# Optimization experiments

Hardware: AMD Instinct MI355X
Metric: run time of the kernel (lower is better)

The kernel has to match this reference:

```python
import jax, jax.numpy as jnp
import numpy as np

NUM_HEADS = 16
HEAD_SIZE = 64
N_EMBD = 1024
BLOCK_SIZE = 2048
B, T = 4, 2048


def setup_inputs() -> dict:
    key = jax.random.key(0)
    ks = jax.random.split(key, 6)
    scale = (N_EMBD * NUM_HEADS) ** (-0.5)
    x = jax.random.normal(ks[0], (B, T, N_EMBD), dtype=jnp.float32)
    Wk = jax.random.normal(ks[1], (NUM_HEADS, N_EMBD, HEAD_SIZE), dtype=jnp.float32) * scale
    Wq = jax.random.normal(ks[2], (NUM_HEADS, N_EMBD, HEAD_SIZE), dtype=jnp.float32) * scale
    Wv = jax.random.normal(ks[3], (NUM_HEADS, N_EMBD, HEAD_SIZE), dtype=jnp.float32) * scale
    proj_w = jax.random.normal(ks[4], (N_EMBD, N_EMBD), dtype=jnp.float32) * (N_EMBD ** -0.5)
    proj_b = jax.random.normal(ks[5], (N_EMBD,), dtype=jnp.float32) * 0.01
    return {"x": x, "Wk": Wk, "Wq": Wq, "Wv": Wv, "proj_w": proj_w, "proj_b": proj_b}


def reference(x, Wk, Wq, Wv, proj_w, proj_b):
    Bsz, Tlen, C = x.shape
    # per-head projections: x [b,t,c] @ W [h,c,d] -> [b,h,t,d]
    q = jnp.einsum('btc,hcd->bhtd', x, Wq)
    k = jnp.einsum('btc,hcd->bhtd', x, Wk)
    v = jnp.einsum('btc,hcd->bhtd', x, Wv)
    wei = jnp.einsum('bhtd,bhsd->bhts', q, k) * (HEAD_SIZE ** -0.5)
    causal = jnp.tril(jnp.ones((Tlen, Tlen), dtype=bool))  # [T,T]
    wei = jnp.where(causal[None, None, :, :], wei, -jnp.inf)
    wei = jax.nn.softmax(wei, axis=-1)
    out = jnp.einsum('bhts,bhsd->bhtd', wei, v)
    out = out.transpose(0, 2, 1, 3).reshape(Bsz, Tlen, NUM_HEADS * HEAD_SIZE)
    out = out @ proj_w.T + proj_b  # nn.Linear: x W^T + b
    return out
```

## Files before the change

### kernel.cpp

```cpp
#include <hip/hip_runtime.h>
#include <hip/hip_bf16.h>

#define BB 4
#define TT 2048
#define CC 1024
#define HH 16
#define DD 64
#define MM (BB * TT)
#define NN_QKV 3072

typedef __attribute__((ext_vector_type(8))) short short8;
typedef __attribute__((ext_vector_type(4))) short short4v;
typedef __attribute__((ext_vector_type(4))) int i32x4;
typedef __attribute__((ext_vector_type(4))) float f32x4;
typedef __attribute__((ext_vector_type(16))) float f32x16;

static __device__ __forceinline__ float exp2_hw(float x) {
  return __builtin_amdgcn_exp2f(x);
}

static __device__ __forceinline__ short f2bf(float f) {
  __hip_bfloat16 h = __float2bfloat16(f);
  short s;
  __builtin_memcpy(&s, &h, 2);
  return s;
}

static __device__ __forceinline__ unsigned int pack2(float a, float b) {
  unsigned int lo = (unsigned short)f2bf(a);
  unsigned int hi = (unsigned short)f2bf(b);
  return lo | (hi << 16);
}

static __device__ __forceinline__ f32x16 zero16() {
  f32x16 z;
#pragma unroll
  for (int i = 0; i < 16; ++i) z[i] = 0.f;
  return z;
}

static __device__ __forceinline__ int swzv(int d) {
  return (((d & 7) ^ ((d >> 3) & 7)) << 4);
}

static __device__ __forceinline__ void gld16(const void* g, void* l) {
  __builtin_amdgcn_global_load_lds(
      (const __attribute__((address_space(1))) unsigned int*)g,
      (__attribute__((address_space(3))) unsigned int*)l, 16, 0, 0);
}

__global__ __launch_bounds__(256) void cvt8_kernel(const float* __restrict__ in,
                                                   short* __restrict__ out, int n8) {
  int i = blockIdx.x * 256 + threadIdx.x;
  if (i >= n8) return;
  const float4 a = ((const float4*)in)[i * 2];
  const float4 b = ((const float4*)in)[i * 2 + 1];
  short8 o;
  o[0] = f2bf(a.x); o[1] = f2bf(a.y); o[2] = f2bf(a.z); o[3] = f2bf(a.w);
  o[4] = f2bf(b.x); o[5] = f2bf(b.y); o[6] = f2bf(b.z); o[7] = f2bf(b.w);
  ((short8*)out)[i] = o;
}

__global__ __launch_bounds__(256) void cvtw_kernel(
    const float* __restrict__ Wq, const float* __restrict__ Wk,
    const float* __restrict__ Wv, short* __restrict__ Wt) {
  __shared__ float tile[64][65];
  const int tid = threadIdx.x;
  const int h = blockIdx.x;
  const int c0 = blockIdx.y * 64;
  const int sel = blockIdx.z;
  const float* W = (sel == 0) ? Wq : (sel == 1) ? Wk : Wv;

#pragma unroll
  for (int it = 0; it < 16; ++it) {
    int e = it * 256 + tid;
    int cc = e >> 6, d = e & 63;
    tile[d][cc] = W[((size_t)h * CC + c0 + cc) * DD + d];
  }
  __syncthreads();
#pragma unroll
  for (int it = 0; it < 16; ++it) {
    int e = it * 256 + tid;
    int d = e >> 6, cc = e & 63;
    Wt[((size_t)((sel * 16 + h) * 64 + d)) * CC + c0 + cc] = f2bf(tile[d][cc]);
  }
}

__global__ __launch_bounds__(512, 2) void qkv256_kernel(
    const short* __restrict__ A, const short* __restrict__ Bt,
    __hip_bfloat16* __restrict__ Oq, __hip_bfloat16* __restrict__ Ok,
    __hip_bfloat16* __restrict__ Ov) {
  __shared__ __align__(16) char LDS[131072];

  const int tid = threadIdx.x;
  const int w = tid >> 6, l = tid & 63;
  const int ll = l & 15, lg = l >> 4;
  const int wm = w >> 2, wn = w & 3;
  const int m0 = blockIdx.x * 256;
  const int n0 = blockIdx.y * 256;

  const int srow = tid >> 3;
  const int schunk = tid & 7;
  const int sswz = (schunk ^ (srow & 7)) * 8;

  f32x4 acc[8][4];
#pragma unroll
  for (int i = 0; i < 8; ++i)
#pragma unroll
    for (int j = 0; j < 4; ++j) acc[i][j] = f32x4{0.f, 0.f, 0.f, 0.f};

#pragma unroll
  for (int i = 0; i < 4; ++i) {
    gld16(A + (size_t)(m0 + i * 64 + srow) * CC + sswz, LDS + i * 8192 + w * 1024);
    gld16(Bt + (size_t)(n0 + i * 64 + srow) * CC + sswz,
          LDS + 32768 + i * 8192 + w * 1024);
  }
  __syncthreads();

  int cur = 0;
#pragma unroll 1
  for (int kt = 0; kt < CC; kt += 64) {
    const char* Ab = LDS + cur * 65536;
    const char* Bb = Ab + 32768;
    const char* nbase_lds = LDS + (cur ^ 1) * 65536;
    const bool haveNext = (kt + 64 < CC);
    const int ktn = kt + 64;

    short8 bfrag[4][2];
#pragma unroll
    for (int p = 0; p < 4; ++p) {
      if (p == 0) {
#pragma unroll
        for (int n = 0; n < 4; ++n) {
          const int rowB = wn * 64 + n * 16 + ll;
#pragma unroll
          for (int k = 0; k < 2; ++k)
            bfrag[n][k] = *(const short8*)(Bb + rowB * 128 +
                                           (((k * 4 + lg) ^ (ll & 7)) * 16));
        }
      }
      short8 afrag[2][2];
#pragma unroll
      for (int i = 0; i < 2; ++i) {
        const int rowA = wm * 128 + (2 * p + i) * 16 + ll;
#pragma unroll
        for (int k = 0; k < 2; ++k)
          afrag[i][k] = *(const short8*)(Ab + rowA * 128 +
                                         (((k * 4 + lg) ^ (ll & 7)) * 16));
      }

      if (haveNext) {
        if (p < 2) {
          const int i0 = p * 2, i1 = p * 2 + 1;
          gld16(A + (size_t)(m0 + i0 * 64 + srow) * CC + ktn + sswz,
                (char*)nbase_lds + i0 * 8192 + w * 1024);
          gld16(A + (size_t)(m0 + i1 * 64 + srow) * CC + ktn + sswz,
                (char*)nbase_lds + i1 * 8192 + w * 1024);
        } else {
          const int i0 = (p - 2) * 2, i1 = (p - 2) * 2 + 1;
          gld16(Bt + (size_t)(n0 + i0 * 64 + srow) * CC + ktn + sswz,
                (char*)nbase_lds + 32768 + i0 * 8192 + w * 1024);
          gld16(Bt + (size_t)(n0 + i1 * 64 + srow) * CC + ktn + sswz,
                (char*)nbase_lds + 32768 + i1 * 8192 + w * 1024);
        }
      }

      __builtin_amdgcn_s_barrier();
      __builtin_amdgcn_s_setprio(1);
#pragma unroll
      for (int i = 0; i < 2; ++i)
#pragma unroll
        for (int n = 0; n < 4; ++n)
#pragma unroll
          for (int k = 0; k < 2; ++k)
            acc[2 * p + i][n] = __builtin_amdgcn_mfma_f32_16x16x32_bf16(
                afrag[i][k], bfrag[n][k], acc[2 * p + i][n], 0, 0, 0);
      __builtin_amdgcn_s_setprio(0);
      if (p < 3) __builtin_amdgcn_s_barrier();
    }

    __syncthreads();
    cur ^= 1;
  }

  const int b = m0 >> 11;
#pragma unroll
  for (int n = 0; n < 4; ++n) {
    const int nbase = n0 + wn * 64 + n * 16;
    const int sel = nbase >> 10;
    const int h = (nbase >> 6) & 15;
    const int d = (nbase & 63) + ll;
    __hip_bfloat16* O = (sel == 0) ? Oq : (sel == 1) ? Ok : Ov;
    const float sc = (sel == 0) ? 0.18033688011112042f : 1.0f;
#pragma unroll
    for (int i = 0; i < 8; ++i) {
#pragma unroll
      for (int r = 0; r < 4; ++r) {
        const int t = (m0 + wm * 128 + i * 16 + lg * 4 + r) & (TT - 1);
        O[(((size_t)b * HH + h) * TT + t) * DD + d] =
            __float2bfloat16(acc[i][n][r] * sc);
      }
    }
  }
}

__global__ __launch_bounds__(256) void proj_gemm_kernel(
    const short* __restrict__ A, const short* __restrict__ Bt,
    const float* __restrict__ bias, float* __restrict__ Of) {
  __shared__ __align__(16) short Als[128 * 32];
  __shared__ __align__(16) short Bls[128 * 32];

  const int tid = threadIdx.x;
  const int w = tid >> 6, l = tid & 63;
  const int lg = l >> 4, ll = l & 15;
  const int wr = w >> 1, wc = w & 1;
  const int m0 = blockIdx.x * 128;
  const int n0 = blockIdx.y * 128;

  const int row0 = tid >> 2, kc0 = (tid & 3) * 8;
  const int row1 = (tid + 256) >> 2, kc1 = (tid & 3) * 8;

  f32x4 acc[4][4] = {};

  for (int kt = 0; kt < CC; kt += 32) {
    __syncthreads();
    gld16(A + (size_t)(m0 + row0) * CC + kt + kc0, (char*)Als + w * 1024);
    gld16(A + (size_t)(m0 + row1) * CC + kt + kc1, (char*)Als + 4096 + w * 1024);
    gld16(Bt + (size_t)(n0 + row0) * CC + kt + kc0, (char*)Bls + w * 1024);
    gld16(Bt + (size_t)(n0 + row1) * CC + kt + kc1, (char*)Bls + 4096 + w * 1024);
    __syncthreads();

    short8 af[4], bfr[4];
#pragma unroll
    for (int i = 0; i < 4; ++i)
      af[i] = *(const short8*)&Als[(wr * 64 + i * 16 + ll) * 32 + lg * 8];
#pragma unroll
    for (int j = 0; j < 4; ++j)
      bfr[j] = *(const short8*)&Bls[(wc * 64 + j * 16 + ll) * 32 + lg * 8];
#pragma unroll
    for (int i = 0; i < 4; ++i)
#pragma unroll
      for (int j = 0; j < 4; ++j)
        acc[i][j] = __builtin_amdgcn_mfma_f32_16x16x32_bf16(af[i], bfr[j], acc[i][j], 0, 0, 0);
  }

#pragma unroll
  for (int j = 0; j < 4; ++j) {
    const int n = n0 + wc * 64 + j * 16 + ll;
    const float bv = bias[n];
#pragma unroll
    for (int i = 0; i < 4; ++i) {
#pragma unroll
      for (int r = 0; r < 4; ++r) {
        const int m = m0 + wr * 64 + i * 16 + lg * 4 + r;
        Of[(size_t)m * CC + n] = acc[i][j][r] + bv;
      }
    }
  }
}

__global__ __launch_bounds__(512) void attn32_kernel(
    const __hip_bfloat16* __restrict__ qg, const __hip_bfloat16* __restrict__ kg,
    const __hip_bfloat16* __restrict__ vg, __hip_bfloat16* __restrict__ att) {
  __shared__ __align__(16) char LDS[34816];
  char* Ks = LDS;
  char* Vt0 = LDS + 16384;
  char* Vt1 = LDS + 24576;

  const int tid = threadIdx.x;
  const int w = tid >> 6, l = tid & 63;
  const int l31 = l & 31, hi = l >> 5;
  const int w4 = w & 3, g = w >> 2;

  const int flat = blockIdx.x;
  const int r_ = flat >> 6;
  const int qt = (r_ < 4) ? (15 - r_) : (r_ < 8) ? (r_ + 4)
               : (r_ < 12) ? (15 - r_) : (r_ - 12);
  const int hb = flat & 63;
  const int h = hb & 15, b = hb >> 4;
  const size_t base = ((size_t)b * HH + h) * TT * DD;

  const int q0w = qt * 128 + w4 * 32;
  const int myq = q0w + l31;

  const short* Kg = (const short*)kg + base;
  const short* Vg = (const short*)vg + base;
  const int kr = tid >> 3;
  const int kc = tid & 7;
  const int vs = tid >> 3;
  const int vd0 = (tid & 7) * 8;

  const short* Qp = (const short*)qg + base + (size_t)myq * DD;
  const short8 qf0 = *(const short8*)(Qp + 0 + hi * 8);
  const short8 qf1 = *(const short8*)(Qp + 16 + hi * 8);
  const short8 qf2 = *(const short8*)(Qp + 32 + hi * 8);
  const short8 qf3 = *(const short8*)(Qp + 48 + hi * 8);

  f32x16 o0 = zero16(), o1 = zero16();
  float lsum = 0.f;

  const int npair = qt + 1;

#pragma unroll 1
  for (int pt = 0; pt < npair; ++pt) {
    const int sb = pt * 128;

    gld16(Kg + (size_t)(sb + kr) * DD + ((kc ^ (kr & 7)) * 8), Ks + w * 1024);
    gld16(Kg + (size_t)(sb + kr + 64) * DD + ((kc ^ (kr & 7)) * 8),
          Ks + 8192 + w * 1024);
    const short8 va = *(const short8*)(Vg + (size_t)(sb + vs) * DD + vd0);
    const short8 vb = *(const short8*)(Vg + (size_t)(sb + 64 + vs) * DD + vd0);
#pragma unroll
    for (int e = 0; e < 8; ++e) {
      const int d = vd0 + e;
      *(short*)(Vt0 + d * 128 + ((vs * 2) ^ swzv(d))) = va[e];
      *(short*)(Vt1 + d * 128 + ((vs * 2) ^ swzv(d))) = vb[e];
    }
    __syncthreads();

    const int sbg = sb + g * 64;
    const char* Vtg = g ? Vt1 : Vt0;
#pragma unroll
    for (int ks = 0; ks < 2; ++ks) {
      const int sbh = sbg + ks * 32;
      if (sbh > q0w + 31) continue;

      const int krow = g * 64 + ks * 32 + l31;
      const char* Kr = Ks + krow * 128;
      const int rsz = (krow & 7) << 4;
      const short8 kf0 = *(const short8*)(Kr + ((0 * 32 + hi * 16) ^ rsz));
      const short8 kf1 = *(const short8*)(Kr + ((1 * 32 + hi * 16) ^ rsz));
      const short8 kf2 = *(const short8*)(Kr + ((2 * 32 + hi * 16) ^ rsz));
      const short8 kf3 = *(const short8*)(Kr + ((3 * 32 + hi * 16) ^ rsz));
      f32x16 sT = zero16();
      __builtin_amdgcn_s_setprio(1);
      sT = __builtin_amdgcn_mfma_f32_32x32x16_bf16(kf0, qf0, sT, 0, 0, 0);
      sT = __builtin_amdgcn_mfma_f32_32x32x16_bf16(kf1, qf1, sT, 0, 0, 0);
      sT = __builtin_amdgcn_mfma_f32_32x32x16_bf16(kf2, qf2, sT, 0, 0, 0);
      sT = __builtin_amdgcn_mfma_f32_32x32x16_bf16(kf3, qf3, sT, 0, 0, 0);
      __builtin_amdgcn_s_setprio(0);

      float p[16];
      if (sbh == q0w) {
#pragma unroll
        for (int r = 0; r < 16; ++r) {
          const int sg = sbh + (r & 3) + 8 * (r >> 2) + 4 * hi;
          p[r] = (sg > myq) ? -INFINITY : sT[r];
        }
      } else {
#pragma unroll
        for (int r = 0; r < 16; ++r) p[r] = sT[r];
      }

      float ps = 0.f;
#pragma unroll
      for (int r = 0; r < 16; ++r) {
        p[r] = exp2_hw(p[r]);
        ps += p[r];
      }
      lsum += ps;

      unsigned int W[4][2], X[4][2];
#pragma unroll
      for (int qd = 0; qd < 4; ++qd) {
        W[qd][0] = pack2(p[4 * qd + 0], p[4 * qd + 1]);
        W[qd][1] = pack2(p[4 * qd + 2], p[4 * qd + 3]);
        X[qd][0] = __shfl_xor((int)W[qd][0], 32);
        X[qd][1] = __shfl_xor((int)W[qd][1], 32);
      }

#pragma unroll
      for (int kst = 0; kst < 2; ++kst) {
        union { i32x4 i; short8 s; } A;
        A.i[0] = hi ? (int)X[2 * kst + 1][0] : (int)W[2 * kst][0];
        A.i[1] = hi ? (int)X[2 * kst + 1][1] : (int)W[2 * kst][1];
        A.i[2] = hi ? (int)W[2 * kst + 1][0] : (int)X[2 * kst][0];
        A.i[3] = hi ? (int)W[2 * kst + 1][1] : (int)X[2 * kst][1];
        const int kb = (ks * 32 + kst * 16 + hi * 8) * 2;
        const int r0 = l31, r1 = 32 + l31;
        const short8 vf0 = *(const short8*)(Vtg + r0 * 128 + (kb ^ swzv(r0)));
        const short8 vf1 = *(const short8*)(Vtg + r1 * 128 + (kb ^ swzv(r1)));
        __builtin_amdgcn_s_setprio(1);
        o0 = __builtin_amdgcn_mfma_f32_32x32x16_bf16(vf0, A.s, o0, 0, 0, 0);
        o1 = __builtin_amdgcn_mfma_f32_32x32x16_bf16(vf1, A.s, o1, 0, 0, 0);
        __builtin_amdgcn_s_setprio(0);
      }
    }
    __syncthreads();
  }

  lsum += __shfl_xor(lsum, 32);

  float* comb = (float*)LDS;
  const int idx17 = (w4 * 64 + l) * 17;
  if (g == 1) {
#pragma unroll
    for (int i = 0; i < 16; ++i) comb[idx17 + i] = o0[i];
    comb[idx17 + 16] = lsum;
  }
  __syncthreads();
  if (g == 0) {
#pragma unroll
    for (int i = 0; i < 16; ++i) o0[i] += comb[idx17 + i];
    lsum += comb[idx17 + 16];
  }
  __syncthreads();
  const int idx16 = (w4 * 64 + l) * 16;
  if (g == 1) {
#pragma unroll
    for (int i = 0; i < 16; ++i) comb[idx16 + i] = o1[i];
  }
  __syncthreads();
  if (g == 0) {
#pragma unroll
    for (int i = 0; i < 16; ++i) o1[i] += comb[idx16 + i];

    const float inv = 1.0f / lsum;
    short* orow = (short*)att + ((size_t)b * TT + myq) * CC + h * DD;
#pragma unroll
    for (int j = 0; j < 4; ++j) {
      short4v s0, s1;
#pragma unroll
      for (int i = 0; i < 4; ++i) {
        s0[i] = f2bf(o0[4 * j + i] * inv);
        s1[i] = f2bf(o1[4 * j + i] * inv);
      }
      *(short4v*)(orow + 8 * j + 4 * hi) = s0;
      *(short4v*)(orow + 32 + 8 * j + 4 * hi) = s1;
    }
  }
}

extern "C" void kernel_launch(void* const* d_in, const int* in_sizes, int n_in,
                              void* d_out, int out_size, void* d_ws, size_t ws_size,
                              hipStream_t stream) {
  const float* x  = (const float*)d_in[0];
  const float* Wk = (const float*)d_in[1];
  const float* Wq = (const float*)d_in[2];
  const float* Wv = (const float*)d_in[3];
  const float* pw = (const float*)d_in[4];
  const float* pb = (const float*)d_in[5];
  float* out = (float*)d_out;

  const size_t QE = (size_t)BB * HH * TT * DD;
  __hip_bfloat16* q   = (__hip_bfloat16*)d_ws;
  __hip_bfloat16* k   = q + QE;
  __hip_bfloat16* v   = k + QE;
  short* xbf          = (short*)(v + QE);
  __hip_bfloat16* att = (__hip_bfloat16*)xbf;
  short* Wt           = xbf + QE;
  short* pwbf         = Wt;

  cvt8_kernel<<<(MM * CC / 8 + 255) / 256, 256, 0, stream>>>(x, xbf, MM * CC / 8);
  cvtw_kernel<<<dim3(HH, CC / 64, 3), 256, 0, stream>>>(Wq, Wk, Wv, Wt);
  qkv256_kernel<<<dim3(MM / 256, NN_QKV / 256), 512, 0, stream>>>(
      xbf, Wt, q, k, v);
  attn32_kernel<<<dim3(1024, 1, 1), 512, 0, stream>>>(q, k, v, att);
  cvt8_kernel<<<(CC * CC / 8 + 255) / 256, 256, 0, stream>>>(pw, pwbf, CC * CC / 8);
  proj_gemm_kernel<<<dim3(MM / 128, CC / 128), 256, 0, stream>>>(
      (const short*)att, pwbf, pb, out);
}
```

Baseline: 166.0 us.

## Reorder QKV GEMM global-to-LDS staging with partial vmcnt waits

Restructures the double-buffered QKV projection GEMM main loop. It issues the B tile loads first and reorders the A row-block loads so the last-needed A blocks arrive last. The full __syncthreads is replaced by explicit s_waitcnt vmcnt(N) waits and barriers, so waves can start on the current tile while some loads are still in flight. The goal is to hide global load latency behind MFMA work. This depends on the vmcnt counting matching the exact load order, which makes it fragile if the compiler adds other vector memory ops.

```diff
diff --git a/kernel.cpp b/kernel.cpp
--- a/kernel.cpp
+++ b/kernel.cpp
@@ -109,63 +109,48 @@
 #pragma unroll
     for (int j = 0; j < 4; ++j) acc[i][j] = f32x4{0.f, 0.f, 0.f, 0.f};
 
-#pragma unroll
-  for (int i = 0; i < 4; ++i) {
-    gld16(A + (size_t)(m0 + i * 64 + srow) * CC + sswz, LDS + i * 8192 + w * 1024);
-    gld16(Bt + (size_t)(n0 + i * 64 + srow) * CC + sswz,
-          LDS + 32768 + i * 8192 + w * 1024);
-  }
-  __syncthreads();
+#define STAGE_A(i, kt, buf) \
+  gld16(A + (size_t)(m0 + (i) * 64 + srow) * CC + (kt) + sswz, \
+        (buf) + (i) * 8192 + w * 1024)
+#define STAGE_B(i, kt, buf) \
+  gld16(Bt + (size_t)(n0 + (i) * 64 + srow) * CC + (kt) + sswz, \
+        (buf) + 32768 + (i) * 8192 + w * 1024)
+
+  STAGE_B(0, 0, LDS); STAGE_B(1, 0, LDS); STAGE_B(2, 0, LDS); STAGE_B(3, 0, LDS);
+  STAGE_A(0, 0, LDS); STAGE_A(2, 0, LDS); STAGE_A(1, 0, LDS); STAGE_A(3, 0, LDS);
 
   int cur = 0;
 #pragma unroll 1
   for (int kt = 0; kt < CC; kt += 64) {
-    const char* Ab = LDS + cur * 65536;
-    const char* Bb = Ab + 32768;
-    const char* nbase_lds = LDS + (cur ^ 1) * 65536;
+    char* Ab = LDS + cur * 65536;
+    char* Bb = Ab + 32768;
+    char* nb = LDS + (cur ^ 1) * 65536;
     const bool haveNext = (kt + 64 < CC);
     const int ktn = kt + 64;
 
+    asm volatile("s_waitcnt vmcnt(2)" ::: "memory");
+    __builtin_amdgcn_s_barrier();
+
     short8 bfrag[4][2];
-#pragma unroll
-    for (int p = 0; p < 4; ++p) {
-      if (p == 0) {
-#pragma unroll
-        for (int n = 0; n < 4; ++n) {
-          const int rowB = wn * 64 + n * 16 + ll;
-#pragma unroll
-          for (int k = 0; k < 2; ++k)
-            bfrag[n][k] = *(const short8*)(Bb + rowB * 128 +
-                                           (((k * 4 + lg) ^ (ll & 7)) * 16));
-        }
-      }
+    if (haveNext) { STAGE_B(0, ktn, nb); STAGE_B(1, ktn, nb); }
+#pragma unroll
+    for (int n = 0; n < 4; ++n) {
+      const int rowB = wn * 64 + n * 16 + ll;
+#pragma unroll
+      for (int k = 0; k < 2; ++k)
+        bfrag[n][k] = *(const short8*)(Bb + rowB * 128 +
+                                       (((k * 4 + lg) ^ (ll & 7)) * 16));
+    }
+    {
       short8 afrag[2][2];
 #pragma unroll
       for (int i = 0; i < 2; ++i) {
-        const int rowA = wm * 128 + (2 * p + i) * 16 + ll;
+        const int rowA = wm * 128 + (0 + i) * 16 + ll;
 #pragma unroll
         for (int k = 0; k < 2; ++k)
           afrag[i][k] = *(const short8*)(Ab + rowA * 128 +
                                          (((k * 4 + lg) ^ (ll & 7)) * 16));
       }
-
-      if (haveNext) {
-        if (p < 2) {
-          const int i0 = p * 2, i1 = p * 2 + 1;
-          gld16(A + (size_t)(m0 + i0 * 64 + srow) * CC + ktn + sswz,
-                (char*)nbase_lds + i0 * 8192 + w * 1024);
-          gld16(A + (size_t)(m0 + i1 * 64 + srow) * CC + ktn + sswz,
-                (char*)nbase_lds + i1 * 8192 + w * 1024);
-        } else {
-          const int i0 = (p - 2) * 2, i1 = (p - 2) * 2 + 1;
-          gld16(Bt + (size_t)(n0 + i0 * 64 + srow) * CC + ktn + sswz,
-                (char*)nbase_lds + 32768 + i0 * 8192 + w * 1024);
-          gld16(Bt + (size_t)(n0 + i1 * 64 + srow) * CC + ktn + sswz,
-                (char*)nbase_lds + 32768 + i1 * 8192 + w * 1024);
-        }
-      }
-
-      __builtin_amdgcn_s_barrier();
       __builtin_amdgcn_s_setprio(1);
 #pragma unroll
       for (int i = 0; i < 2; ++i)
@@ -173,15 +158,92 @@
         for (int n = 0; n < 4; ++n)
 #pragma unroll
           for (int k = 0; k < 2; ++k)
-            acc[2 * p + i][n] = __builtin_amdgcn_mfma_f32_16x16x32_bf16(
-                afrag[i][k], bfrag[n][k], acc[2 * p + i][n], 0, 0, 0);
+            acc[i][n] = __builtin_amdgcn_mfma_f32_16x16x32_bf16(
+                afrag[i][k], bfrag[n][k], acc[i][n], 0, 0, 0);
       __builtin_amdgcn_s_setprio(0);
-      if (p < 3) __builtin_amdgcn_s_barrier();
-    }
-
-    __syncthreads();
+    }
+    __builtin_amdgcn_s_barrier();
+
+    if (haveNext) { STAGE_B(2, ktn, nb); STAGE_B(3, ktn, nb); }
+    {
+      short8 afrag[2][2];
+#pragma unroll
+      for (int i = 0; i < 2; ++i) {
+        const int rowA = wm * 128 + (2 + i) * 16 + ll;
+#pragma unroll
+        for (int k = 0; k < 2; ++k)
+          afrag[i][k] = *(const short8*)(Ab + rowA * 128 +
+                                         (((k * 4 + lg) ^ (ll & 7)) * 16));
+      }
+      __builtin_amdgcn_s_setprio(1);
+#pragma unroll
+      for (int i = 0; i < 2; ++i)
+#pragma unroll
+        for (int n = 0; n < 4; ++n)
+#pragma unroll
+          for (int k = 0; k < 2; ++k)
+            acc[2 + i][n] = __builtin_amdgcn_mfma_f32_16x16x32_bf16(
+                afrag[i][k], bfrag[n][k], acc[2 + i][n], 0, 0, 0);
+      __builtin_amdgcn_s_setprio(0);
+    }
+    __builtin_amdgcn_s_barrier();
+
+    if (haveNext) {
+      STAGE_A(0, ktn, nb); STAGE_A(2, ktn, nb);
+      asm volatile("s_waitcnt vmcnt(6)" ::: "memory");
+    } else {
+      asm volatile("s_waitcnt vmcnt(0)" ::: "memory");
+    }
+    __builtin_amdgcn_s_barrier();
+    {
+      short8 afrag[2][2];
+#pragma unroll
+      for (int i = 0; i < 2; ++i) {
+        const int rowA = wm * 128 + (4 + i) * 16 + ll;
+#pragma unroll
+        for (int k = 0; k < 2; ++k)
+          afrag[i][k] = *(const short8*)(Ab + rowA * 128 +
+                                         (((k * 4 + lg) ^ (ll & 7)) * 16));
+      }
+      __builtin_amdgcn_s_setprio(1);
+#pragma unroll
+      for (int i = 0; i < 2; ++i)
+#pragma unroll
+        for (int n = 0; n < 4; ++n)
+#pragma unroll
+          for (int k = 0; k < 2; ++k)
+            acc[4 + i][n] = __builtin_amdgcn_mfma_f32_16x16x32_bf16(
+                afrag[i][k], bfrag[n][k], acc[4 + i][n], 0, 0, 0);
+      __builtin_amdgcn_s_setprio(0);
+    }
+    __builtin_amdgcn_s_barrier();
+
+    if (haveNext) { STAGE_A(1, ktn, nb); STAGE_A(3, ktn, nb); }
+    {
+      short8 afrag[2][2];
+#pragma unroll
+      for (int i = 0; i < 2; ++i) {
+        const int rowA = wm * 128 + (6 + i) * 16 + ll;
+#pragma unroll
+        for (int k = 0; k < 2; ++k)
+          afrag[i][k] = *(const short8*)(Ab + rowA * 128 +
+                                         (((k * 4 + lg) ^ (ll & 7)) * 16));
+      }
+      __builtin_amdgcn_s_setprio(1);
+#pragma unroll
+      for (int i = 0; i < 2; ++i)
+#pragma unroll
+        for (int n = 0; n < 4; ++n)
+#pragma unroll
+          for (int k = 0; k < 2; ++k)
+            acc[6 + i][n] = __builtin_amdgcn_mfma_f32_16x16x32_bf16(
+                afrag[i][k], bfrag[n][k], acc[6 + i][n], 0, 0, 0);
+      __builtin_amdgcn_s_setprio(0);
+    }
     cur ^= 1;
   }
+#undef STAGE_A
+#undef STAGE_B
 
   const int b = m0 >> 11;
 #pragma unroll
```

After: 162.6 us. -2.1%, faster.
